# Optimization experiments

Measured on AMD Instinct MI355X. Metric: run time of the kernel, lower is better.

## Reference

```python
import jax, jax.numpy as jnp
import numpy as np
import math

DIM = 384
NH = 6
DH = DIM // NH
B = 2
S = 2048
EPS = 1e-6
LN_EPS = 1e-5


def setup_inputs() -> dict:
    key = jax.random.key(0)
    ks = jax.random.split(key, 8)
    q = jax.random.normal(ks[0], (B, S, DIM), dtype=jnp.float32)
    k = jax.random.normal(ks[1], (B, S, DIM), dtype=jnp.float32)
    v = jax.random.normal(ks[2], (B, S, DIM), dtype=jnp.float32)
    # gate linear params (Linear(3*dim, num_heads)); small random weights to exercise the math
    igate_w = jax.random.normal(ks[3], (NH, 3 * DIM), dtype=jnp.float32) * 0.02
    igate_b = jax.random.normal(ks[4], (NH,), dtype=jnp.float32) * 0.1
    fgate_w = jax.random.normal(ks[5], (NH, 3 * DIM), dtype=jnp.float32) * 0.02
    fgate_b = jnp.linspace(3.0, 6.0, NH, dtype=jnp.float32)
    # MultiHeadLayerNorm residual weight (stored as delta, effective scale = 1 + w)
    outnorm_weight = jax.random.normal(ks[6], (DIM,), dtype=jnp.float32) * 0.02
    return {"q": q, "k": k, "v": v, "igate_w": igate_w, "igate_b": igate_b,
            "fgate_w": fgate_w, "fgate_b": fgate_b, "outnorm_weight": outnorm_weight}


def _mlstm_forward(q, k, v, igate_w, igate_b, fgate_w, fgate_b, outnorm_weight):
    Bq, Sq, _ = q.shape
    gate_in = jnp.concatenate([q, k, v], axis=-1)                       # (B,S,3D)
    ig = gate_in @ igate_w.T + igate_b                                   # (B,S,NH)
    fg = gate_in @ fgate_w.T + fgate_b                                   # (B,S,NH)
    # split heads: (B,NH,S,DH)
    qh = q.reshape(Bq, Sq, NH, DH).transpose(0, 2, 1, 3)
    kh = k.reshape(Bq, Sq, NH, DH).transpose(0, 2, 1, 3)
    vh = v.reshape(Bq, Sq, NH, DH).transpose(0, 2, 1, 3)
    ig = ig.transpose(0, 2, 1)                                           # (B,NH,S)
    fg = fg.transpose(0, 2, 1)                                           # (B,NH,S)

    log_fg = jax.nn.log_sigmoid(fg)                                      # (B,NH,S)
    lfc = jnp.concatenate([jnp.zeros((Bq, NH, 1), dtype=q.dtype),
                           jnp.cumsum(log_fg, axis=-1)], axis=-1)        # (B,NH,S+1)
    # log_fg_matrix[i,j] = cumsum[i] - cumsum[j] (sliced [1:,1:]), masked causal
    diff = lfc[:, :, 1:, None] - lfc[:, :, None, 1:]                     # (B,NH,S,S)
    ltr = jnp.tril(jnp.ones((Sq, Sq), dtype=bool))
    log_fg_mat = jnp.where(ltr, diff, -jnp.inf)
    log_D = log_fg_mat + ig[:, :, None, :]                               # + igate^T
    max_log_D = jnp.max(log_D, axis=-1, keepdims=True)                   # rowwise stabilize
    D = jnp.exp(log_D - max_log_D)
    qk = jnp.einsum('bhsd,bhtd->bhst', qh, kh) / math.sqrt(DH)
    C = qk * D
    normalizer = jnp.maximum(jnp.abs(jnp.sum(C, axis=-1, keepdims=True)),
                             jnp.exp(-max_log_D))
    h = jnp.einsum('bhst,bhtd->bhsd', C / (normalizer + EPS), vh)        # (B,NH,S,DH)

    # MultiHeadLayerNorm == group_norm over each head's DH channels, scale=(1+w)
    mean = jnp.mean(h, axis=-1, keepdims=True)
    var = jnp.var(h, axis=-1, keepdims=True)
    normed = (h - mean) / jnp.sqrt(var + LN_EPS)
    scale = (1.0 + outnorm_weight).reshape(NH, DH)[None, :, None, :]
    out = normed * scale
    return out.transpose(0, 2, 1, 3).reshape(Bq, Sq, DIM)


def reference(q, k, v, igate_w, igate_b, fgate_w, fgate_b, outnorm_weight):
    return _mlstm_forward(q, k, v, igate_w, igate_b, fgate_w, fgate_b, outnorm_weight)
```

## Files before the change

### kernel.cpp

```cpp
#include <hip/hip_runtime.h>
#include <math.h>

#define DIM 384
#define NH 6
#define DH 64
#define B_ 2
#define S_ 2048
#define EPS 1e-6f
#define LN_EPS 1e-5f
#define G3 (3*DIM)
#define LOG2E 1.44269504f
#define KSTR 72
#define NT (S_/64)
#define NSPLIT 4
#define NBH (B_*NH)

typedef __attribute__((ext_vector_type(8))) short bf16x8;
typedef __attribute__((ext_vector_type(4))) short bf16x4;
typedef __attribute__((ext_vector_type(4))) float f32x4;
typedef __attribute__((ext_vector_type(8))) unsigned short u16x8;

__device__ __forceinline__ unsigned short f2bf(float f){
    unsigned int u = __float_as_uint(f);
    u += 0x7fff + ((u >> 16) & 1);
    return (unsigned short)(u >> 16);
}
__device__ __forceinline__ float bf2f(unsigned short u){
    return __uint_as_float(((unsigned int)u) << 16);
}
__device__ __forceinline__ float logsig(float x){
    return fminf(x, 0.f) - log1pf(expf(-fabsf(x)));
}

__global__ __launch_bounds__(256) void cvt_kernel(
    const float* __restrict__ q, const float* __restrict__ k, const float* __restrict__ v,
    unsigned short* __restrict__ Qb, unsigned short* __restrict__ Kb,
    unsigned short* __restrict__ Vt) {
    __shared__ unsigned short lt[64*KSTR];
    int bh = blockIdx.y;
    int b = bh / NH, h = bh % NH;
    int t0 = blockIdx.x * 64;
    int tid = threadIdx.x;
    #pragma unroll
    for (int i = 0; i < 4; i++){
        int idx = tid + 256*i;
        int r = idx >> 4;
        int c4 = (idx & 15) * 4;
        size_t off = ((size_t)b*S_ + t0 + r)*DIM + h*DH + c4;
        float4 xq = *(const float4*)(q + off);
        ushort4 tq; tq.x=f2bf(xq.x*0.125f); tq.y=f2bf(xq.y*0.125f);
        tq.z=f2bf(xq.z*0.125f); tq.w=f2bf(xq.w*0.125f);
        *(ushort4*)(Qb + off) = tq;
        float4 xk = *(const float4*)(k + off);
        ushort4 tk; tk.x=f2bf(xk.x); tk.y=f2bf(xk.y); tk.z=f2bf(xk.z); tk.w=f2bf(xk.w);
        *(ushort4*)(Kb + off) = tk;
        float4 xv = *(const float4*)(v + off);
        lt[(c4+0)*KSTR + r] = f2bf(xv.x);
        lt[(c4+1)*KSTR + r] = f2bf(xv.y);
        lt[(c4+2)*KSTR + r] = f2bf(xv.z);
        lt[(c4+3)*KSTR + r] = f2bf(xv.w);
    }
    __syncthreads();
    #pragma unroll
    for (int i = 0; i < 2; i++){
        int idx = tid + 256*i;
        int d = idx >> 3;
        int t8 = (idx & 7) * 8;
        u16x8 o = *(const u16x8*)&lt[d*KSTR + t8];
        *(u16x8*)(Vt + (size_t)bh*DH*S_ + (size_t)d*S_ + t0 + t8) = o;
    }
}

__global__ __launch_bounds__(256) void gates_kernel(
    const float* __restrict__ q, const float* __restrict__ k, const float* __restrict__ v,
    const float* __restrict__ iw, const float* __restrict__ ib,
    const float* __restrict__ fw, const float* __restrict__ fb,
    float* __restrict__ ig_out, float* __restrict__ lf_out) {
    int wave = (blockIdx.x * 256 + threadIdx.x) >> 6;
    int lane = threadIdx.x & 63;
    int b = wave / S_, s = wave % S_;
    size_t base = ((size_t)b * S_ + s) * DIM;
    float aI[NH], aF[NH];
    #pragma unroll
    for (int h = 0; h < NH; h++){ aI[h] = 0.f; aF[h] = 0.f; }
    for (int g = lane; g < G3/4; g += 64) {
        int e = g * 4;
        float4 x4;
        if (e < DIM)        x4 = *(const float4*)(q + base + e);
        else if (e < 2*DIM) x4 = *(const float4*)(k + base + e - DIM);
        else                x4 = *(const float4*)(v + base + e - 2*DIM);
        #pragma unroll
        for (int h = 0; h < NH; h++){
            float4 wi = *(const float4*)(iw + h*G3 + e);
            float4 wf = *(const float4*)(fw + h*G3 + e);
            aI[h] = fmaf(x4.x, wi.x, fmaf(x4.y, wi.y, fmaf(x4.z, wi.z, fmaf(x4.w, wi.w, aI[h]))));
            aF[h] = fmaf(x4.x, wf.x, fmaf(x4.y, wf.y, fmaf(x4.z, wf.z, fmaf(x4.w, wf.w, aF[h]))));
        }
    }
    #pragma unroll
    for (int h = 0; h < NH; h++){
        #pragma unroll
        for (int off = 32; off >= 1; off >>= 1){
            aI[h] += __shfl_xor(aI[h], off, 64);
            aF[h] += __shfl_xor(aF[h], off, 64);
        }
    }
    if (lane == 0) {
        #pragma unroll
        for (int h = 0; h < NH; h++){
            ig_out[((size_t)b*NH + h)*S_ + s] = aI[h] + ib[h];
            lf_out[((size_t)b*NH + h)*S_ + s] = logsig(aF[h] + fb[h]);
        }
    }
}

__global__ __launch_bounds__(256) void scan_kernel(
    const float* __restrict__ lf, const float* __restrict__ ig,
    float* __restrict__ cum, float* __restrict__ e2, float* __restrict__ pm,
    float* __restrict__ me, float* __restrict__ baseA){
    int bh = blockIdx.x;
    const float* srcL = lf + (size_t)bh * S_;
    const float* srcI = ig + (size_t)bh * S_;
    float* dstC = cum + (size_t)bh * S_;
    float* dstE = e2 + (size_t)bh * S_;
    float* dstP = pm + (size_t)bh * S_;
    int tid = threadIdx.x;
    float loc[8];
    float run = 0.f;
    #pragma unroll
    for (int j = 0; j < 8; j++){ run += srcL[tid*8 + j]; loc[j] = run; }
    __shared__ float sm[256];
    sm[tid] = run;
    __syncthreads();
    float total = run;
    for (int off = 1; off < 256; off <<= 1){
        float vv = (tid >= off) ? sm[tid - off] : 0.f;
        __syncthreads();
        sm[tid] += vv;
        __syncthreads();
    }
    float excl = sm[tid] - total;
    float c[8];
    #pragma unroll
    for (int j = 0; j < 8; j++){ c[j] = excl + loc[j]; dstC[tid*8 + j] = c[j]; }
    __shared__ float sb[32];
    if ((tid & 7) == 0) sb[tid >> 3] = excl;
    __syncthreads();
    float base_t = sb[tid >> 3];
    float E[8], mloc = -INFINITY;
    #pragma unroll
    for (int j = 0; j < 8; j++){
        E[j] = srcI[tid*8 + j] - c[j] + base_t;
        dstE[tid*8 + j] = exp2f(E[j] * LOG2E);
        mloc = fmaxf(mloc, E[j]);
    }
    __shared__ float smax[256];
    smax[tid] = mloc;
    __syncthreads();
    float carry = -INFINITY;
    int g0 = tid & ~7;
    for (int u = g0; u < tid; u++) carry = fmaxf(carry, smax[u]);
    float runm = carry;
    #pragma unroll
    for (int j = 0; j < 8; j++){
        runm = fmaxf(runm, E[j]);
        dstP[tid*8 + j] = runm;
    }
    if ((tid & 7) == 7) me[bh*NT + (tid >> 3)] = runm;
    if ((tid & 7) == 0) baseA[bh*NT + (tid >> 3)] = base_t;
}

__global__ __launch_bounds__(256) void mlstm_part(
    const unsigned short* __restrict__ Qb, const unsigned short* __restrict__ Kb,
    const unsigned short* __restrict__ Vt,
    const float* __restrict__ cum, const float* __restrict__ e2,
    const float* __restrict__ pm, const float* __restrict__ me,
    const float* __restrict__ baseA,
    unsigned short* __restrict__ pOb, float* __restrict__ pM, float* __restrict__ pL) {
    int lin = blockIdx.x;
    int sp  = lin / NBH;
    int bh  = lin % NBH;
    int st  = (NT - 1) - (sp >> 2);
    int c   = sp & 3;
    int L   = (st + 4) >> 2;
    int tb0 = c * L;
    int tb1 = min((c + 1) * L, st + 1);
    int pblk = lin;
    int tid = threadIdx.x;

    if (tb0 >= tb1){
        if (tid < 64){ pM[pblk*64 + tid] = -INFINITY; pL[pblk*64 + tid] = 0.f; }
        return;
    }

    __shared__ unsigned short kt[64*KSTR];
    __shared__ unsigned short vt[64*KSTR];

    int b = bh / NH, h = bh % NH;
    int s0 = st * 64;
    int wv   = tid >> 6;
    int lane = tid & 63;
    int lq   = lane & 15;
    int quad = lane >> 4;

    const unsigned short* kbT = Kb + (size_t)b*S_*DIM + h*DH;
    const unsigned short* vtB = Vt + (size_t)bh*DH*S_;
    const float* cmb = cum + (size_t)bh*S_;
    const float* e2b = e2 + (size_t)bh*S_;
    const float* meB = me + bh*NT;
    const float* baseB = baseA + bh*NT;

    int s_glob = s0 + 16*wv + lq;

    bf16x8 qf[2];
    {
        const unsigned short* qr = Qb + ((size_t)b*S_ + s_glob)*DIM + h*DH;
        qf[0] = *(const bf16x8*)(qr + 8*quad);
        qf[1] = *(const bf16x8*)(qr + 32 + 8*quad);
    }

    float cq   = cmb[s_glob];
    float pm_s = pm[(size_t)bh*S_ + s_glob];
    float m_s = -INFINITY, b_s = 0.f;
    f32x4 oacc[4];
    #pragma unroll
    for (int cg = 0; cg < 4; cg++) oacc[cg] = (f32x4){0.f,0.f,0.f,0.f};

    int sr[2], sc[2];
    #pragma unroll
    for (int i = 0; i < 2; i++){
        int idx = tid + 256*i;
        sr[i] = idx >> 3;
        sc[i] = (idx & 7) * 8;
    }

    u16x8 kreg[2], vreg[2];
    {
        const unsigned short* kb = kbT + (size_t)(tb0*64)*DIM;
        const unsigned short* vb = vtB + tb0*64;
        #pragma unroll
        for (int i = 0; i < 2; i++){
            kreg[i] = *(const u16x8*)(kb + (size_t)sr[i]*DIM + sc[i]);
            vreg[i] = *(const u16x8*)(vb + (size_t)sr[i]*S_ + sc[i]);
        }
    }

    for (int t0 = tb0*64; t0 < tb1*64; t0 += 64){
        int tix = t0 >> 6;
        float base_t = baseB[tix];
        float me_t   = meB[tix];
        float4 e2v[4];
        #pragma unroll
        for (int tb = 0; tb < 4; tb++)
            e2v[tb] = *(const float4*)(e2b + t0 + 16*tb + 4*quad);

        __syncthreads();
        #pragma unroll
        for (int i = 0; i < 2; i++){
            *(u16x8*)&kt[sr[i]*KSTR + sc[i]] = kreg[i];
            *(u16x8*)&vt[sr[i]*KSTR + sc[i]] = vreg[i];
        }
        __syncthreads();

        if (t0 + 64 < tb1*64){
            const unsigned short* kb = kbT + (size_t)(t0 + 64)*DIM;
            const unsigned short* vb = vtB + (t0 + 64);
            #pragma unroll
            for (int i = 0; i < 2; i++){
                kreg[i] = *(const u16x8*)(kb + (size_t)sr[i]*DIM + sc[i]);
                vreg[i] = *(const u16x8*)(vb + (size_t)sr[i]*S_ + sc[i]);
            }
        }

        f32x4 st4[4];
        #pragma unroll
        for (int tb = 0; tb < 4; tb++) st4[tb] = (f32x4){0.f,0.f,0.f,0.f};
        #pragma unroll
        for (int ks = 0; ks < 2; ks++){
            #pragma unroll
            for (int tb = 0; tb < 4; tb++){
                bf16x8 af = *(const bf16x8*)&kt[(16*tb + lq)*KSTR + 32*ks + 8*quad];
                st4[tb] = __builtin_amdgcn_mfma_f32_16x16x32_bf16(af, qf[ks], st4[tb], 0, 0, 0);
            }
        }

        bool diag = (t0 == s0);
        float A = cq - base_t;
        float pmax = A + (diag ? pm_s : me_t);
        float mn = fmaxf(m_s, pmax);
        float sc2 = exp2f((m_s - mn) * LOG2E);
        float ws = exp2f((A - mn) * LOG2E);
        m_s = mn;
        float pv[4][4];
        #pragma unroll
        for (int tb = 0; tb < 4; tb++){
            #pragma unroll
            for (int r = 0; r < 4; r++)
                pv[tb][r] = st4[tb][r] * (ws * e2v[tb][r]);
        }
        if (diag){
            #pragma unroll
            for (int tb = 0; tb < 4; tb++){
                #pragma unroll
                for (int r = 0; r < 4; r++)
                    if (t0 + 16*tb + 4*quad + r > s_glob) pv[tb][r] = 0.f;
            }
        }
        float rs = 0.f;
        bf16x4 pf[4];
        #pragma unroll
        for (int tb = 0; tb < 4; tb++){
            #pragma unroll
            for (int r = 0; r < 4; r++){
                rs += pv[tb][r];
                pf[tb][r] = (short)f2bf(pv[tb][r]);
            }
        }
        rs += __shfl_xor(rs, 16, 64);
        rs += __shfl_xor(rs, 32, 64);
        b_s = b_s * sc2 + rs;

        #pragma unroll
        for (int r = 0; r < 4; r++){
            float sco = __shfl(sc2, 20*quad + r, 64);
            #pragma unroll
            for (int cg = 0; cg < 4; cg++) oacc[cg][r] *= sco;
        }

        #pragma unroll
        for (int tb = 0; tb < 4; tb++){
            #pragma unroll
            for (int cg = 0; cg < 4; cg++){
                bf16x4 vf = *(const bf16x4*)&vt[(16*cg + lq)*KSTR + 16*tb + 4*quad];
                oacc[cg] = __builtin_amdgcn_mfma_f32_16x16x16bf16_1k(pf[tb], vf, oacc[cg], 0, 0, 0);
            }
        }
    }

    unsigned short* po = pOb + (size_t)pblk * 4096;
    #pragma unroll
    for (int r = 0; r < 4; r++){
        int row = 16*wv + 4*quad + r;
        #pragma unroll
        for (int cg = 0; cg < 4; cg++)
            po[row*64 + 16*cg + lq] = f2bf(oacc[cg][r]);
    }
    if (quad == 0){
        pM[pblk*64 + 16*wv + lq] = m_s;
        pL[pblk*64 + 16*wv + lq] = b_s;
    }
}

__global__ __launch_bounds__(256) void mlstm_combine(
    const unsigned short* __restrict__ pOb, const float* __restrict__ pM,
    const float* __restrict__ pL, const float* __restrict__ w,
    float* __restrict__ out) {
    int st = blockIdx.x;
    int bh = blockIdx.y;
    int b = bh / NH, h = bh % NH;
    int tid = threadIdx.x;
    int cl = (tid & 15) * 4;
    int rb = tid >> 4;

    int pblk[NSPLIT];
    #pragma unroll
    for (int p = 0; p < NSPLIT; p++)
        pblk[p] = (((NT - 1 - st) << 2) + p) * NBH + bh;

    float4 wv4 = *(const float4*)(w + h*DH + cl);

    #pragma unroll
    for (int pass = 0; pass < 4; pass++){
        int row = pass*16 + rb;
        float mp[NSPLIT], lp[NSPLIT];
        float mmax = -INFINITY;
        #pragma unroll
        for (int p = 0; p < NSPLIT; p++){
            mp[p] = pM[pblk[p]*64 + row];
            lp[p] = pL[pblk[p]*64 + row];
            mmax = fmaxf(mmax, mp[p]);
        }
        float l = 0.f;
        float ox = 0.f, oy = 0.f, oz = 0.f, ow = 0.f;
        #pragma unroll
        for (int p = 0; p < NSPLIT; p++){
            if (mp[p] != -INFINITY){
                float wp = exp2f((mp[p] - mmax) * LOG2E);
                l += wp * lp[p];
                ushort4 t4 = *(const ushort4*)(pOb + (size_t)pblk[p]*4096 + row*64 + cl);
                ox += wp*bf2f(t4.x); oy += wp*bf2f(t4.y);
                oz += wp*bf2f(t4.z); ow += wp*bf2f(t4.w);
            }
        }
        float nrm = fmaxf(fabsf(l), exp2f(-mmax * LOG2E));
        float inv = 1.f / (nrm + EPS);
        float x[4] = {ox*inv, oy*inv, oz*inv, ow*inv};
        float s1 = x[0]+x[1]+x[2]+x[3];
        float s2 = x[0]*x[0]+x[1]*x[1]+x[2]*x[2]+x[3]*x[3];
        #pragma unroll
        for (int off = 8; off >= 1; off >>= 1){
            s1 += __shfl_xor(s1, off, 64);
            s2 += __shfl_xor(s2, off, 64);
        }
        float mean = s1 * (1.f/64.f);
        float var  = s2 * (1.f/64.f) - mean*mean;
        float rstd = rsqrtf(var + LN_EPS);
        float4 oo;
        oo.x = (x[0]-mean)*rstd*(1.f + wv4.x);
        oo.y = (x[1]-mean)*rstd*(1.f + wv4.y);
        oo.z = (x[2]-mean)*rstd*(1.f + wv4.z);
        oo.w = (x[3]-mean)*rstd*(1.f + wv4.w);
        *(float4*)(out + ((size_t)b*S_ + st*64 + row)*DIM + h*DH + cl) = oo;
    }
}

extern "C" void kernel_launch(void* const* d_in, const int* in_sizes, int n_in,
                              void* d_out, int out_size, void* d_ws, size_t ws_size,
                              hipStream_t stream) {
    const float* q  = (const float*)d_in[0];
    const float* k  = (const float*)d_in[1];
    const float* v  = (const float*)d_in[2];
    const float* iw = (const float*)d_in[3];
    const float* ib = (const float*)d_in[4];
    const float* fw = (const float*)d_in[5];
    const float* fb = (const float*)d_in[6];
    const float* w  = (const float*)d_in[7];
    float* out = (float*)d_out;

    const int nPart = NBH * NT * NSPLIT;
    const size_t NE = (size_t)B_ * S_ * DIM;
    float* ig   = (float*)d_ws;
    float* lf   = ig   + (size_t)NBH*S_;
    float* cum  = lf   + (size_t)NBH*S_;
    float* e2   = cum  + (size_t)NBH*S_;
    float* pm   = e2   + (size_t)NBH*S_;
    float* me   = pm   + (size_t)NBH*S_;
    float* base = me   + (size_t)NBH*NT;
    float* pM   = base + (size_t)NBH*NT;
    float* pL   = pM   + (size_t)nPart*64;
    unsigned short* pOb = (unsigned short*)(pL + (size_t)nPart*64);
    unsigned short* Qb  = pOb + (size_t)nPart*4096;
    unsigned short* Kb  = Qb + NE;
    unsigned short* Vt  = Kb + NE;

    cvt_kernel<<<dim3(NT, NBH), 256, 0, stream>>>(q, k, v, Qb, Kb, Vt);
    gates_kernel<<<B_*S_/4, 256, 0, stream>>>(q, k, v, iw, ib, fw, fb, ig, lf);
    scan_kernel<<<NBH, 256, 0, stream>>>(lf, ig, cum, e2, pm, me, base);
    mlstm_part<<<nPart, 256, 0, stream>>>(Qb, Kb, Vt, cum, e2, pm, me, base, pOb, pM, pL);
    mlstm_combine<<<dim3(NT, NBH), 256, 0, stream>>>(pOb, pM, pL, w, out);
}
```

Measured before the change: 134.1 us.

## Fuse Q/K bf16 conversion into gates kernel; load K/V fragments directly from global

Q and K bf16 conversion moves into the gates kernel, which already reads q and k, so the separate conversion pass only transposes V. In the attention partial kernel, the LDS staging of K and V tiles and the two barriers per tile are removed. Each wave instead loads its MFMA operand fragments straight from global memory into registers. This trades LDS traffic and synchronisation for redundant global/L2 reads across the four waves, uncoalesced strided loads, and higher register pressure.

```diff
diff --git a/kernel.cpp b/kernel.cpp
--- a/kernel.cpp
+++ b/kernel.cpp
@@ -32,10 +32,8 @@
     return fminf(x, 0.f) - log1pf(expf(-fabsf(x)));
 }
 
-__global__ __launch_bounds__(256) void cvt_kernel(
-    const float* __restrict__ q, const float* __restrict__ k, const float* __restrict__ v,
-    unsigned short* __restrict__ Qb, unsigned short* __restrict__ Kb,
-    unsigned short* __restrict__ Vt) {
+__global__ __launch_bounds__(256) void vt_kernel(
+    const float* __restrict__ v, unsigned short* __restrict__ Vt) {
     __shared__ unsigned short lt[64*KSTR];
     int bh = blockIdx.y;
     int b = bh / NH, h = bh % NH;
@@ -46,19 +44,11 @@
         int idx = tid + 256*i;
         int r = idx >> 4;
         int c4 = (idx & 15) * 4;
-        size_t off = ((size_t)b*S_ + t0 + r)*DIM + h*DH + c4;
-        float4 xq = *(const float4*)(q + off);
-        ushort4 tq; tq.x=f2bf(xq.x*0.125f); tq.y=f2bf(xq.y*0.125f);
-        tq.z=f2bf(xq.z*0.125f); tq.w=f2bf(xq.w*0.125f);
-        *(ushort4*)(Qb + off) = tq;
-        float4 xk = *(const float4*)(k + off);
-        ushort4 tk; tk.x=f2bf(xk.x); tk.y=f2bf(xk.y); tk.z=f2bf(xk.z); tk.w=f2bf(xk.w);
-        *(ushort4*)(Kb + off) = tk;
-        float4 xv = *(const float4*)(v + off);
-        lt[(c4+0)*KSTR + r] = f2bf(xv.x);
-        lt[(c4+1)*KSTR + r] = f2bf(xv.y);
-        lt[(c4+2)*KSTR + r] = f2bf(xv.z);
-        lt[(c4+3)*KSTR + r] = f2bf(xv.w);
+        float4 x = *(const float4*)(v + ((size_t)b*S_ + t0 + r)*DIM + h*DH + c4);
+        lt[(c4+0)*KSTR + r] = f2bf(x.x);
+        lt[(c4+1)*KSTR + r] = f2bf(x.y);
+        lt[(c4+2)*KSTR + r] = f2bf(x.z);
+        lt[(c4+3)*KSTR + r] = f2bf(x.w);
     }
     __syncthreads();
     #pragma unroll
@@ -75,7 +65,8 @@
     const float* __restrict__ q, const float* __restrict__ k, const float* __restrict__ v,
     const float* __restrict__ iw, const float* __restrict__ ib,
     const float* __restrict__ fw, const float* __restrict__ fb,
-    float* __restrict__ ig_out, float* __restrict__ lf_out) {
+    float* __restrict__ ig_out, float* __restrict__ lf_out,
+    unsigned short* __restrict__ Qb, unsigned short* __restrict__ Kb) {
     int wave = (blockIdx.x * 256 + threadIdx.x) >> 6;
     int lane = threadIdx.x & 63;
     int b = wave / S_, s = wave % S_;
@@ -86,9 +77,18 @@
     for (int g = lane; g < G3/4; g += 64) {
         int e = g * 4;
         float4 x4;
-        if (e < DIM)        x4 = *(const float4*)(q + base + e);
-        else if (e < 2*DIM) x4 = *(const float4*)(k + base + e - DIM);
-        else                x4 = *(const float4*)(v + base + e - 2*DIM);
+        if (e < DIM){
+            x4 = *(const float4*)(q + base + e);
+            ushort4 t; t.x=f2bf(x4.x*0.125f); t.y=f2bf(x4.y*0.125f);
+            t.z=f2bf(x4.z*0.125f); t.w=f2bf(x4.w*0.125f);
+            *(ushort4*)(Qb + base + e) = t;
+        } else if (e < 2*DIM){
+            x4 = *(const float4*)(k + base + e - DIM);
+            ushort4 t; t.x=f2bf(x4.x); t.y=f2bf(x4.y); t.z=f2bf(x4.z); t.w=f2bf(x4.w);
+            *(ushort4*)(Kb + base + e - DIM) = t;
+        } else {
+            x4 = *(const float4*)(v + base + e - 2*DIM);
+        }
         #pragma unroll
         for (int h = 0; h < NH; h++){
             float4 wi = *(const float4*)(iw + h*G3 + e);
@@ -193,9 +193,6 @@
         return;
     }
 
-    __shared__ unsigned short kt[64*KSTR];
-    __shared__ unsigned short vt[64*KSTR];
-
     int b = bh / NH, h = bh % NH;
     int s0 = st * 64;
     int wv   = tid >> 6;
@@ -226,26 +223,21 @@
     #pragma unroll
     for (int cg = 0; cg < 4; cg++) oacc[cg] = (f32x4){0.f,0.f,0.f,0.f};
 
-    int sr[2], sc[2];
-    #pragma unroll
-    for (int i = 0; i < 2; i++){
-        int idx = tid + 256*i;
-        sr[i] = idx >> 3;
-        sc[i] = (idx & 7) * 8;
-    }
-
-    u16x8 kreg[2], vreg[2];
-    {
-        const unsigned short* kb = kbT + (size_t)(tb0*64)*DIM;
-        const unsigned short* vb = vtB + tb0*64;
-        #pragma unroll
-        for (int i = 0; i < 2; i++){
-            kreg[i] = *(const u16x8*)(kb + (size_t)sr[i]*DIM + sc[i]);
-            vreg[i] = *(const u16x8*)(vb + (size_t)sr[i]*S_ + sc[i]);
-        }
-    }
-
     for (int t0 = tb0*64; t0 < tb1*64; t0 += 64){
+        const unsigned short* kR = kbT + (size_t)t0*DIM;
+        bf16x8 af[2][4];
+        #pragma unroll
+        for (int ks = 0; ks < 2; ks++)
+            #pragma unroll
+            for (int tb = 0; tb < 4; tb++)
+                af[ks][tb] = *(const bf16x8*)(kR + (size_t)(16*tb + lq)*DIM + 32*ks + 8*quad);
+        bf16x4 vf[4][4];
+        #pragma unroll
+        for (int tb = 0; tb < 4; tb++)
+            #pragma unroll
+            for (int cg = 0; cg < 4; cg++)
+                vf[tb][cg] = *(const bf16x4*)(vtB + (size_t)(16*cg + lq)*S_ + t0 + 16*tb + 4*quad);
+
         int tix = t0 >> 6;
         float base_t = baseB[tix];
         float me_t   = meB[tix];
@@ -254,35 +246,14 @@
         for (int tb = 0; tb < 4; tb++)
             e2v[tb] = *(const float4*)(e2b + t0 + 16*tb + 4*quad);
 
-        __syncthreads();
-        #pragma unroll
-        for (int i = 0; i < 2; i++){
-            *(u16x8*)&kt[sr[i]*KSTR + sc[i]] = kreg[i];
-            *(u16x8*)&vt[sr[i]*KSTR + sc[i]] = vreg[i];
-        }
-        __syncthreads();
-
-        if (t0 + 64 < tb1*64){
-            const unsigned short* kb = kbT + (size_t)(t0 + 64)*DIM;
-            const unsigned short* vb = vtB + (t0 + 64);
-            #pragma unroll
-            for (int i = 0; i < 2; i++){
-                kreg[i] = *(const u16x8*)(kb + (size_t)sr[i]*DIM + sc[i]);
-                vreg[i] = *(const u16x8*)(vb + (size_t)sr[i]*S_ + sc[i]);
-            }
-        }
-
         f32x4 st4[4];
         #pragma unroll
         for (int tb = 0; tb < 4; tb++) st4[tb] = (f32x4){0.f,0.f,0.f,0.f};
         #pragma unroll
-        for (int ks = 0; ks < 2; ks++){
-            #pragma unroll
-            for (int tb = 0; tb < 4; tb++){
-                bf16x8 af = *(const bf16x8*)&kt[(16*tb + lq)*KSTR + 32*ks + 8*quad];
-                st4[tb] = __builtin_amdgcn_mfma_f32_16x16x32_bf16(af, qf[ks], st4[tb], 0, 0, 0);
-            }
-        }
+        for (int ks = 0; ks < 2; ks++)
+            #pragma unroll
+            for (int tb = 0; tb < 4; tb++)
+                st4[tb] = __builtin_amdgcn_mfma_f32_16x16x32_bf16(af[ks][tb], qf[ks], st4[tb], 0, 0, 0);
 
         bool diag = (t0 == s0);
         float A = cq - base_t;
@@ -293,18 +264,16 @@
         m_s = mn;
         float pv[4][4];
         #pragma unroll
-        for (int tb = 0; tb < 4; tb++){
+        for (int tb = 0; tb < 4; tb++)
             #pragma unroll
             for (int r = 0; r < 4; r++)
                 pv[tb][r] = st4[tb][r] * (ws * e2v[tb][r]);
-        }
         if (diag){
             #pragma unroll
-            for (int tb = 0; tb < 4; tb++){
+            for (int tb = 0; tb < 4; tb++)
                 #pragma unroll
                 for (int r = 0; r < 4; r++)
                     if (t0 + 16*tb + 4*quad + r > s_glob) pv[tb][r] = 0.f;
-            }
         }
         float rs = 0.f;
         bf16x4 pf[4];
@@ -328,13 +297,10 @@
         }
 
         #pragma unroll
-        for (int tb = 0; tb < 4; tb++){
-            #pragma unroll
-            for (int cg = 0; cg < 4; cg++){
-                bf16x4 vf = *(const bf16x4*)&vt[(16*cg + lq)*KSTR + 16*tb + 4*quad];
-                oacc[cg] = __builtin_amdgcn_mfma_f32_16x16x16bf16_1k(pf[tb], vf, oacc[cg], 0, 0, 0);
-            }
-        }
+        for (int tb = 0; tb < 4; tb++)
+            #pragma unroll
+            for (int cg = 0; cg < 4; cg++)
+                oacc[cg] = __builtin_amdgcn_mfma_f32_16x16x16bf16_1k(pf[tb], vf[tb][cg], oacc[cg], 0, 0, 0);
     }
 
     unsigned short* po = pOb + (size_t)pblk * 4096;
@@ -443,8 +409,8 @@
     unsigned short* Kb  = Qb + NE;
     unsigned short* Vt  = Kb + NE;
 
-    cvt_kernel<<<dim3(NT, NBH), 256, 0, stream>>>(q, k, v, Qb, Kb, Vt);
-    gates_kernel<<<B_*S_/4, 256, 0, stream>>>(q, k, v, iw, ib, fw, fb, ig, lf);
+    vt_kernel<<<dim3(NT, NBH), 256, 0, stream>>>(v, Vt);
+    gates_kernel<<<B_*S_/4, 256, 0, stream>>>(q, k, v, iw, ib, fw, fb, ig, lf, Qb, Kb);
     scan_kernel<<<NBH, 256, 0, stream>>>(lf, ig, cum, e2, pm, me, base);
     mlstm_part<<<nPart, 256, 0, stream>>>(Qb, Kb, Vt, cum, e2, pm, me, base, pOb, pM, pL);
     mlstm_combine<<<dim3(NT, NBH), 256, 0, stream>>>(pOb, pM, pL, w, out);
```

Result: slower. 193.4 us (+44.2%).
